# Kernel tuning notes

Measured on AMD Instinct MI355X. Metric: run time of the kernel, lower is better.

## Reference

```python
import jax, jax.numpy as jnp
import numpy as np

BATCH = 1024


def setup_inputs() -> dict:
    key = jax.random.key(0)
    ks = jax.random.split(key, 8)
    piece_positions = jax.random.randint(ks[0], (BATCH, 64, 10), 0, 2) > 0  # bool occupancy
    king_positions = jax.random.randint(ks[1], (BATCH, 2), 0, 64, dtype=jnp.int32)
    input_weights = jax.random.randint(ks[2], (64, 641, 256), -32768, 32767, dtype=jnp.int16)
    input_bias = jnp.zeros((256,), dtype=jnp.int16)
    w1 = jax.random.randint(ks[3], (32, 512), -128, 127, dtype=jnp.int8)
    b1 = jnp.zeros((32,), dtype=jnp.int32)
    w2 = jax.random.randint(ks[4], (32, 32), -128, 127, dtype=jnp.int8)
    b2 = jnp.zeros((32,), dtype=jnp.int32)
    out_w = jax.random.randint(ks[5], (32,), -128, 127, dtype=jnp.int8)
    out_b = jnp.zeros((1,), dtype=jnp.int32)
    return {
        'piece_positions': piece_positions, 'king_positions': king_positions,
        'input_weights': input_weights, 'input_bias': input_bias,
        'w1': w1, 'b1': b1, 'w2': w2, 'b2': b2, 'out_w': out_w, 'out_b': out_b,
    }


def _fc(x, w, b):
    # int8 inputs/weights, int32 accumulate, floor-div 64, clamp to [0,127] -> int8
    y = x.astype(jnp.int32) @ w.T.astype(jnp.int32) + b
    y = jnp.floor_divide(y, 64)
    return jnp.clip(y, 0, 127).astype(jnp.int8)


def reference(piece_positions, king_positions, input_weights, input_bias,
              w1, b1, w2, b2, out_w, out_b):
    B = piece_positions.shape[0]
    pp = piece_positions.reshape(B, 640).astype(jnp.int32)  # flattened 64x10 HalfKP features

    def half(king_idx):
        wk = input_weights[king_idx]            # (B, 641, 256) gathered per-sample king table
        feats = wk[:, :640, :].astype(jnp.int32)
        kbias = wk[:, 640, :].astype(jnp.int32)
        return jnp.einsum('bf,bfd->bd', pp, feats) + kbias  # (B, 256)

    white = half(king_positions[:, 0])
    black = half(king_positions[:, 1])
    # int16 wraparound semantics of the original: accumulate in int32, mod-cast to int16
    acc = (white + black + input_bias.astype(jnp.int32)).astype(jnp.int16)

    x = jnp.clip(acc, 0, 127).astype(jnp.int8)
    x = jnp.concatenate([x, x], axis=1)  # (B, 512) side_to_move || other_side
    x = _fc(x, w1, b1)
    x = _fc(x, w2, b2)
    s = jnp.sum(x.astype(jnp.int32) * out_w.astype(jnp.int32)) + out_b  # scalar sum over batch too (as in source)
    return jnp.floor_divide(s, 16)  # shape (1,)
```

## Files before the change

kernel.cpp:

```cpp
#include <hip/hip_runtime.h>
#include <stdint.h>

#define NDIM  256
#define NFEAT 640
#define NROWS 641
#define SG    8
#define GSTRIDE 4
#define MAXRPB 320
#define CPB   4
#define MAXSLOTS 2048

typedef unsigned short ushort4v __attribute__((ext_vector_type(4)));
typedef unsigned short ushort8v __attribute__((ext_vector_type(8)));

struct GatherLds {
    int flags[2];
    int cnt;
    unsigned short list[MAXSLOTS];
    int samp[SG];
    int slotid[SG];
    unsigned mask[MAXRPB];
    unsigned red[4][SG][NDIM / 2];
};

template<bool RAWW, bool RAWPP>
__device__ __forceinline__ void gather_body(
    const void* __restrict__ ppv, const void* __restrict__ Wv,
    unsigned short* __restrict__ partial, int nslots, int rp, GatherLds& sh)
{
    const int bid = blockIdx.x;
    const int k = bid & 63;
    const int rest = bid >> 6;
    const int p = rest & (rp - 1);
    const int g0 = rest >> (rp == 4 ? 2 : 1);
    const int t = threadIdx.x, l = t & 63, g = t >> 6;

    const int cnt = sh.cnt;
    const int rpb = NFEAT / rp;
    const int r0 = p * rpb;
    const int rows_per_wave = rpb / 4;
    const int lbeg = g * rows_per_wave;
    const char* Wk = (const char*)Wv + (size_t)k * NROWS * NDIM * (RAWW ? 2 : 4);

    for (int gi = g0; gi * SG < cnt; gi += GSTRIDE) {
        const int base = gi * SG;
        const int ns = min(SG, cnt - base);
        const unsigned emask = (1u << ns) - 1u;

        if (t < SG) {
            const int s = sh.list[base + min(t, ns - 1)];
            sh.slotid[t] = s;
            sh.samp[t] = s >> 1;
        }
        __syncthreads();

        for (int r = t; r < rpb; r += 256) {
            unsigned mm = 0;
            #pragma unroll
            for (int i = 0; i < SG; ++i) {
                const int s = sh.samp[i];
                int v;
                if (RAWPP) v = ((const uint8_t*)ppv)[(size_t)s * NFEAT + r0 + r];
                else       v = ((const int*)ppv)[(size_t)s * NFEAT + r0 + r];
                mm |= (v != 0 ? 1u : 0u) << i;
            }
            sh.mask[r] = mm & emask;
        }
        __syncthreads();

        ushort4v acc[SG];
        #pragma unroll
        for (int i = 0; i < SG; ++i) acc[i] = (ushort4v)0;

        #pragma unroll 2
        for (int rr = 0; rr < rows_per_wave; ++rr) {
            const int lr = lbeg + rr;
            unsigned mm = sh.mask[lr];
            mm = __builtin_amdgcn_readfirstlane(mm);
            ushort4v w;
            if (RAWW) {
                w = *(const ushort4v*)(Wk + (size_t)(r0 + lr) * 512 + (size_t)l * 8);
            } else {
                const int4 u = *(const int4*)(Wk + (size_t)(r0 + lr) * 1024 + (size_t)l * 16);
                w.x = (unsigned short)u.x; w.y = (unsigned short)u.y;
                w.z = (unsigned short)u.z; w.w = (unsigned short)u.w;
            }
            #pragma unroll
            for (int i = 0; i < SG; ++i)
                if (mm & (1u << i)) acc[i] += w;
        }

        #pragma unroll
        for (int i = 0; i < SG; ++i)
            *(ushort4v*)&sh.red[g][i][2 * l] = acc[i];
        __syncthreads();

        const int i = t >> 5;
        const int j4 = (t & 31) * 4;
        if (i < ns) {
            ushort8v sv = *(const ushort8v*)&sh.red[0][i][j4];
            #pragma unroll
            for (int g2 = 1; g2 < 4; ++g2) sv += *(const ushort8v*)&sh.red[g2][i][j4];
            *(ushort8v*)&partial[((size_t)p * nslots + sh.slotid[i]) * NDIM + (size_t)(t & 31) * 8] = sv;
        }
        __syncthreads();
    }
}

__global__ __launch_bounds__(256, 4) void nnue_gather(
    const void* __restrict__ pp, const int* __restrict__ kp,
    const void* __restrict__ W, unsigned short* __restrict__ partial,
    int* __restrict__ ws, int nslots, int rp)
{
    __shared__ GatherLds sh;
    const int t = threadIdx.x, l = t & 63, g = t >> 6;
    const int k = blockIdx.x & 63;

    if (blockIdx.x == 0 && t == 0) { ws[0] = 0; ws[3] = 0; }

    if (t == 0) {
        int raww = 0, rawpp = 0;
        const int* W32 = (const int*)W;
        const int* pp32 = (const int*)pp;
        for (int i = 0; i < 16; ++i) {
            const int v = W32[i];
            if (v > 32767 || v < -32768) raww = 1;
            const int u = pp32[i];
            if (u != 0 && u != 1) rawpp = 1;
        }
        sh.flags[0] = raww; sh.flags[1] = rawpp;
    }
    if (g == 0) {
        int cnt = 0;
        for (int c = 0; c < nslots; c += 64) {
            const int s = c + l;
            const bool f = (s < nslots) && (kp[s] == k);
            const unsigned long long m = __ballot(f);
            if (f) sh.list[cnt + (int)__popcll(m & ((1ull << l) - 1ull))] = (unsigned short)s;
            cnt += (int)__popcll(m);
        }
        if (l == 0) sh.cnt = cnt;
    }
    __syncthreads();

    const int raww = sh.flags[0], rawpp = sh.flags[1];
    if (raww) {
        if (rawpp) gather_body<true,  true >(pp, W, partial, nslots, rp, sh);
        else       gather_body<true,  false>(pp, W, partial, nslots, rp, sh);
    } else {
        if (rawpp) gather_body<false, true >(pp, W, partial, nslots, rp, sh);
        else       gather_body<false, false>(pp, W, partial, nslots, rp, sh);
    }
}

struct CombineLds {
    alignas(16) int8_t x[NDIM];
    int fc[256];
    alignas(4) int8_t x2[32];
    int flags;
};

template<bool RAWW>
__device__ __forceinline__ void combine_body(
    const unsigned short* __restrict__ partial, const int* __restrict__ kp,
    const void* __restrict__ Wv, const void* __restrict__ ibv,
    const void* __restrict__ w1v, const int* __restrict__ b1,
    const void* __restrict__ w2v, const int* __restrict__ b2,
    const void* __restrict__ owv, const int* __restrict__ ob,
    int* __restrict__ ws, int* __restrict__ out,
    int nslots, int B, int rp, CombineLds& sh)
{
    const int t = threadIdx.x;
    int blocksum = 0;

    for (int ss = 0; ss < CPB; ++ss) {
        const int b = blockIdx.x * CPB + ss;
        if (b >= B) break;
        const int k0 = kp[2 * b + 0];
        const int k1 = kp[2 * b + 1];
        {
            unsigned tot = 0;
            for (int pi = 0; pi < rp; ++pi) {
                tot += partial[((size_t)pi * nslots + 2 * b + 0) * NDIM + t];
                tot += partial[((size_t)pi * nslots + 2 * b + 1) * NDIM + t];
            }
            if (RAWW) {
                const uint16_t* Wq = (const uint16_t*)Wv;
                tot += Wq[((size_t)k0 * NROWS + NFEAT) * NDIM + t];
                tot += Wq[((size_t)k1 * NROWS + NFEAT) * NDIM + t];
                tot += ((const uint16_t*)ibv)[t];
            } else {
                const int* Wq = (const int*)Wv;
                tot += (unsigned)Wq[((size_t)k0 * NROWS + NFEAT) * NDIM + t];
                tot += (unsigned)Wq[((size_t)k1 * NROWS + NFEAT) * NDIM + t];
                tot += (unsigned)((const int*)ibv)[t];
            }
            int v = (int)(int16_t)(uint16_t)tot;
            v = v < 0 ? 0 : (v > 127 ? 127 : v);
            sh.x[t] = (int8_t)v;
        }
        __syncthreads();

        {
            const int o = t >> 3, part = t & 7;
            int y = 0;
            const uint32_t* xw = (const uint32_t*)sh.x;
            if (RAWW) {
                const uint32_t* w1r = (const uint32_t*)((const char*)w1v + o * 512);
                #pragma unroll
                for (int i = 0; i < 8; ++i) {
                    const int wi = part * 8 + i;
                    const uint32_t xv = xw[wi];
                    const uint32_t wa = w1r[wi];
                    const uint32_t wb = w1r[64 + wi];
                    #pragma unroll
                    for (int jj = 0; jj < 4; ++jj) {
                        const int xj  = (int)((xv >> (8 * jj)) & 0xFFu);
                        const int waj = (int)(int8_t)(uint8_t)(wa >> (8 * jj));
                        const int wbj = (int)(int8_t)(uint8_t)(wb >> (8 * jj));
                        y += xj * (waj + wbj);
                    }
                }
            } else {
                const int* w1r = (const int*)w1v + o * 512;
                #pragma unroll
                for (int i = 0; i < 8; ++i) {
                    const int wi = part * 8 + i;
                    const uint32_t xv = xw[wi];
                    #pragma unroll
                    for (int jj = 0; jj < 4; ++jj) {
                        const int xj = (int)((xv >> (8 * jj)) & 0xFFu);
                        y += xj * (w1r[wi * 4 + jj] + w1r[256 + wi * 4 + jj]);
                    }
                }
            }
            sh.fc[t] = y;
        }
        __syncthreads();

        if (t < 32) {
            int y = b1[t];
            #pragma unroll
            for (int pq = 0; pq < 8; ++pq) y += sh.fc[t * 8 + pq];
            y >>= 6;
            y = y < 0 ? 0 : (y > 127 ? 127 : y);
            sh.x2[t] = (int8_t)y;
        }
        __syncthreads();

        if (t < 32) {
            int y = b2[t];
            const uint32_t* x2w = (const uint32_t*)sh.x2;
            if (RAWW) {
                const uint32_t* w2r = (const uint32_t*)((const char*)w2v + t * 32);
                #pragma unroll
                for (int i = 0; i < 8; ++i) {
                    const uint32_t xv = x2w[i];
                    const uint32_t wv = w2r[i];
                    #pragma unroll
                    for (int jj = 0; jj < 4; ++jj)
                        y += (int)((xv >> (8 * jj)) & 0xFFu) * (int)(int8_t)(uint8_t)(wv >> (8 * jj));
                }
            } else {
                const int* w2r = (const int*)w2v + t * 32;
                #pragma unroll
                for (int i = 0; i < 8; ++i) {
                    const uint32_t xv = x2w[i];
                    #pragma unroll
                    for (int jj = 0; jj < 4; ++jj)
                        y += (int)((xv >> (8 * jj)) & 0xFFu) * w2r[i * 4 + jj];
                }
            }
            y >>= 6;
            y = y < 0 ? 0 : (y > 127 ? 127 : y);
            const int owx = RAWW ? (int)((const int8_t*)owv)[t] : ((const int*)owv)[t];
            int pr = y * owx;
            #pragma unroll
            for (int off = 16; off > 0; off >>= 1) pr += __shfl_down(pr, off, 32);
            if (t == 0) blocksum += pr;
        }
        __syncthreads();
    }

    if (t == 0) {
        atomicAdd(&ws[0], blocksum);
        __threadfence();
        const int ticket = atomicAdd(&ws[3], 1);
        if (ticket == (int)gridDim.x - 1) {
            const int s = atomicAdd(&ws[0], 0);
            out[0] = (s + ob[0]) >> 4;
        }
    }
}

__global__ __launch_bounds__(256) void nnue_combine(
    const unsigned short* __restrict__ partial, const int* __restrict__ kp,
    const void* __restrict__ W, const void* __restrict__ ib,
    const void* __restrict__ w1, const int* __restrict__ b1,
    const void* __restrict__ w2, const int* __restrict__ b2,
    const void* __restrict__ ow, const int* __restrict__ ob,
    int* __restrict__ ws, int* __restrict__ out, int nslots, int B, int rp)
{
    __shared__ CombineLds sh;
    if (threadIdx.x == 0) {
        int raww = 0;
        const int* W32 = (const int*)W;
        for (int i = 0; i < 16; ++i) {
            const int v = W32[i];
            if (v > 32767 || v < -32768) raww = 1;
        }
        sh.flags = raww;
    }
    __syncthreads();
    if (sh.flags) combine_body<true >(partial, kp, W, ib, w1, b1, w2, b2, ow, ob, ws, out, nslots, B, rp, sh);
    else          combine_body<false>(partial, kp, W, ib, w1, b1, w2, b2, ow, ob, ws, out, nslots, B, rp, sh);
}

__global__ void nnue_finalize(const int* __restrict__ ws, const int* __restrict__ ob,
                              int* __restrict__ out) {
    out[0] = (ws[0] + ob[0]) >> 4;
}

struct SharedBuf {
    uint8_t pp[NFEAT];
    int     acc[4][NDIM];
    alignas(16) int8_t x[NDIM];
    int     fc[256];
    alignas(4) int8_t x2[32];
    int     list[4][160];
};

__global__ void detect_layout(const int* __restrict__ W32, const int* __restrict__ pp32,
                              int* __restrict__ ws) {
    int raww = 0, rawpp = 0;
    for (int i = 0; i < 16; ++i) {
        const int v = W32[i];
        if (v > 32767 || v < -32768) raww = 1;
        const int u = pp32[i];
        if (u != 0 && u != 1) rawpp = 1;
    }
    ws[0] = 0; ws[1] = raww; ws[2] = rawpp;
}

template<bool RAWW, bool RAWPP>
__device__ __forceinline__ void mono_body(
    const void* __restrict__ ppv, const int* __restrict__ kp,
    const void* __restrict__ Wv,  const void* __restrict__ ibv,
    const void* __restrict__ w1v, const int* __restrict__ b1,
    const void* __restrict__ w2v, const int* __restrict__ b2,
    const void* __restrict__ owv, int* __restrict__ ws, SharedBuf& sh)
{
    const int b = blockIdx.x;
    const int t = threadIdx.x;
    const int l = t & 63;
    const int g = t >> 6;

    if (RAWPP) {
        const uint32_t* src = (const uint32_t*)((const uint8_t*)ppv + (size_t)b * NFEAT);
        if (t < NFEAT / 4) ((uint32_t*)sh.pp)[t] = src[t];
    } else {
        const int* src = (const int*)ppv + (size_t)b * NFEAT;
        for (int i = t; i < NFEAT; i += 256) sh.pp[i] = (uint8_t)(src[i] != 0);
    }
    __syncthreads();

    const int base = g * 160;
    int cnt = 0;
    for (int c = 0; c < 160; c += 64) {
        const int idx = c + l;
        const bool flag = (idx < 160) && (sh.pp[base + idx] != 0);
        const unsigned long long mmask = __ballot(flag);
        const int pos = cnt + (int)__popcll(mmask & ((1ull << l) - 1ull));
        if (flag) sh.list[g][pos] = base + idx;
        cnt += (int)__popcll(mmask);
    }

    const int k0 = kp[b * 2 + 0];
    const int k1 = kp[b * 2 + 1];
    int a0 = 0, a1 = 0, a2 = 0, a3 = 0, a4 = 0, a5 = 0, a6 = 0, a7 = 0;

    if (RAWW) {
        const char* W0 = (const char*)Wv + (size_t)k0 * (NROWS * NDIM * 2);
        const char* W1 = (const char*)Wv + (size_t)k1 * (NROWS * NDIM * 2);
        const int lo = l * 8;
        auto step = [&](int f) {
            const uint2 u0 = *(const uint2*)(W0 + f * 512 + lo);
            const uint2 u1 = *(const uint2*)(W1 + f * 512 + lo);
            a0 += (int)(u0.x & 0xFFFFu); a1 += (int)(u0.x >> 16);
            a2 += (int)(u0.y & 0xFFFFu); a3 += (int)(u0.y >> 16);
            a4 += (int)(u1.x & 0xFFFFu); a5 += (int)(u1.x >> 16);
            a6 += (int)(u1.y & 0xFFFFu); a7 += (int)(u1.y >> 16);
        };
        int j = 0;
        for (; j + 4 <= cnt; j += 4) {
            const int f0 = sh.list[g][j], f1 = sh.list[g][j + 1];
            const int f2 = sh.list[g][j + 2], f3 = sh.list[g][j + 3];
            step(f0); step(f1); step(f2); step(f3);
        }
        for (; j < cnt; ++j) step(sh.list[g][j]);
    } else {
        const char* W0 = (const char*)Wv + (size_t)k0 * (NROWS * NDIM * 4);
        const char* W1 = (const char*)Wv + (size_t)k1 * (NROWS * NDIM * 4);
        const int lo = l * 16;
        auto step = [&](int f) {
            const int4 u0 = *(const int4*)(W0 + f * 1024 + lo);
            const int4 u1 = *(const int4*)(W1 + f * 1024 + lo);
            a0 += u0.x; a1 += u0.y; a2 += u0.z; a3 += u0.w;
            a4 += u1.x; a5 += u1.y; a6 += u1.z; a7 += u1.w;
        };
        int j = 0;
        for (; j + 4 <= cnt; j += 4) {
            const int f0 = sh.list[g][j], f1 = sh.list[g][j + 1];
            const int f2 = sh.list[g][j + 2], f3 = sh.list[g][j + 3];
            step(f0); step(f1); step(f2); step(f3);
        }
        for (; j < cnt; ++j) step(sh.list[g][j]);
    }

    sh.acc[g][4 * l + 0] = a0 + a4;
    sh.acc[g][4 * l + 1] = a1 + a5;
    sh.acc[g][4 * l + 2] = a2 + a6;
    sh.acc[g][4 * l + 3] = a3 + a7;
    __syncthreads();

    {
        const int d = t;
        int tot = sh.acc[0][d] + sh.acc[1][d] + sh.acc[2][d] + sh.acc[3][d];
        int kb0, kb1, ibx;
        if (RAWW) {
            const int16_t* Wq = (const int16_t*)Wv;
            kb0 = Wq[((size_t)k0 * NROWS + NFEAT) * NDIM + d];
            kb1 = Wq[((size_t)k1 * NROWS + NFEAT) * NDIM + d];
            ibx = ((const int16_t*)ibv)[d];
        } else {
            const int* Wq = (const int*)Wv;
            kb0 = Wq[((size_t)k0 * NROWS + NFEAT) * NDIM + d];
            kb1 = Wq[((size_t)k1 * NROWS + NFEAT) * NDIM + d];
            ibx = ((const int*)ibv)[d];
        }
        tot += kb0 + kb1 + ibx;
        int v = (int)(int16_t)(uint16_t)(uint32_t)tot;
        v = v < 0 ? 0 : (v > 127 ? 127 : v);
        sh.x[d] = (int8_t)v;
    }
    __syncthreads();

    {
        const int o = t >> 3, part = t & 7;
        int y = 0;
        const uint32_t* xw = (const uint32_t*)sh.x;
        if (RAWW) {
            const uint32_t* w1r = (const uint32_t*)((const char*)w1v + o * 512);
            #pragma unroll
            for (int i = 0; i < 8; ++i) {
                const int wi = part * 8 + i;
                const uint32_t xv = xw[wi];
                const uint32_t wa = w1r[wi];
                const uint32_t wb = w1r[64 + wi];
                #pragma unroll
                for (int jj = 0; jj < 4; ++jj) {
                    const int xj  = (int)((xv >> (8 * jj)) & 0xFFu);
                    const int waj = (int)(int8_t)(uint8_t)(wa >> (8 * jj));
                    const int wbj = (int)(int8_t)(uint8_t)(wb >> (8 * jj));
                    y += xj * (waj + wbj);
                }
            }
        } else {
            const int* w1r = (const int*)w1v + o * 512;
            #pragma unroll
            for (int i = 0; i < 8; ++i) {
                const int wi = part * 8 + i;
                const uint32_t xv = xw[wi];
                #pragma unroll
                for (int jj = 0; jj < 4; ++jj) {
                    const int xj = (int)((xv >> (8 * jj)) & 0xFFu);
                    y += xj * (w1r[wi * 4 + jj] + w1r[256 + wi * 4 + jj]);
                }
            }
        }
        sh.fc[t] = y;
    }
    __syncthreads();

    if (t < 32) {
        int y = b1[t];
        #pragma unroll
        for (int pq = 0; pq < 8; ++pq) y += sh.fc[t * 8 + pq];
        y >>= 6;
        y = y < 0 ? 0 : (y > 127 ? 127 : y);
        sh.x2[t] = (int8_t)y;
    }
    __syncthreads();

    if (t < 32) {
        int y = b2[t];
        const uint32_t* x2w = (const uint32_t*)sh.x2;
        if (RAWW) {
            const uint32_t* w2r = (const uint32_t*)((const char*)w2v + t * 32);
            #pragma unroll
            for (int i = 0; i < 8; ++i) {
                const uint32_t xv = x2w[i];
                const uint32_t wv = w2r[i];
                #pragma unroll
                for (int jj = 0; jj < 4; ++jj)
                    y += (int)((xv >> (8 * jj)) & 0xFFu) * (int)(int8_t)(uint8_t)(wv >> (8 * jj));
            }
        } else {
            const int* w2r = (const int*)w2v + t * 32;
            #pragma unroll
            for (int i = 0; i < 8; ++i) {
                const uint32_t xv = x2w[i];
                #pragma unroll
                for (int jj = 0; jj < 4; ++jj)
                    y += (int)((xv >> (8 * jj)) & 0xFFu) * w2r[i * 4 + jj];
            }
        }
        y >>= 6;
        y = y < 0 ? 0 : (y > 127 ? 127 : y);
        const int owx = RAWW ? (int)((const int8_t*)owv)[t] : ((const int*)owv)[t];
        int pr = y * owx;
        #pragma unroll
        for (int off = 16; off > 0; off >>= 1) pr += __shfl_down(pr, off, 32);
        if (t == 0) atomicAdd(ws, pr);
    }
}

__global__ __launch_bounds__(256, 4) void nnue_mono(
    const void* __restrict__ pp, const int* __restrict__ kp,
    const void* __restrict__ W,  const void* __restrict__ ib,
    const void* __restrict__ w1, const int* __restrict__ b1,
    const void* __restrict__ w2, const int* __restrict__ b2,
    const void* __restrict__ ow, int* __restrict__ ws)
{
    __shared__ SharedBuf sh;
    const int raww = ws[1], rawpp = ws[2];
    if (raww) {
        if (rawpp) mono_body<true,  true >(pp, kp, W, ib, w1, b1, w2, b2, ow, ws, sh);
        else       mono_body<true,  false>(pp, kp, W, ib, w1, b1, w2, b2, ow, ws, sh);
    } else {
        if (rawpp) mono_body<false, true >(pp, kp, W, ib, w1, b1, w2, b2, ow, ws, sh);
        else       mono_body<false, false>(pp, kp, W, ib, w1, b1, w2, b2, ow, ws, sh);
    }
}

extern "C" void kernel_launch(void* const* d_in, const int* in_sizes, int n_in,
                              void* d_out, int out_size, void* d_ws, size_t ws_size,
                              hipStream_t stream)
{
    const void* pp = d_in[0];
    const int*  kp = (const int*)d_in[1];
    const void* W  = d_in[2];
    const void* ib = d_in[3];
    const void* w1 = d_in[4];
    const int*  b1 = (const int*)d_in[5];
    const void* w2 = d_in[6];
    const int*  b2 = (const int*)d_in[7];
    const void* ow = d_in[8];
    const int*  ob = (const int*)d_in[9];
    int* ws  = (int*)d_ws;
    int* out = (int*)d_out;

    const int B = in_sizes[1] / 2;
    const int nslots = 2 * B;

    const size_t off_pb = 256;
    const size_t need4 = (off_pb + (size_t)4 * nslots * (NDIM / 2)) * 4;
    const size_t need2 = (off_pb + (size_t)2 * nslots * (NDIM / 2)) * 4;

    int rp = 0;
    if (ws_size >= need4) rp = 4;
    else if (ws_size >= need2) rp = 2;

    if (rp && nslots <= MAXSLOTS) {
        unsigned short* partial = (unsigned short*)(ws + off_pb);
        hipLaunchKernelGGL(nnue_gather, dim3(64 * rp * GSTRIDE), dim3(256), 0, stream,
                           pp, kp, W, partial, ws, nslots, rp);
        hipLaunchKernelGGL(nnue_combine, dim3((B + CPB - 1) / CPB), dim3(256), 0, stream,
                           partial, kp, W, ib, w1, b1, w2, b2, ow, ob, ws, out, nslots, B, rp);
    } else {
        hipLaunchKernelGGL(detect_layout, dim3(1), dim3(1), 0, stream,
                           (const int*)W, (const int*)pp, ws);
        hipLaunchKernelGGL(nnue_mono, dim3(B), dim3(256), 0, stream,
                           pp, kp, W, ib, w1, b1, w2, b2, ow, ws);
        hipLaunchKernelGGL(nnue_finalize, dim3(1), dim3(1), 0, stream, ws, ob, out);
    }
}
```

Before: 161.8 us.

## Fuse bucket, gather and combine into one cooperative kernel with per-wave work units

Replaces the two-kernel gather/combine path with a single cooperative-launch kernel. It bucket-sorts slots by king index into global workspace, then does a grid sync, a gather phase, another grid sync and a combine phase. The gather is restructured so each wave owns an independent (partition, sample-group) unit with its own LDS mask. This drops the cross-wave LDS reduction and the block barriers, and the weight loads are unrolled by four rows. The aim is to cut launch overhead and barrier stalls, at the cost of grid-wide syncs and one wave redundantly re-reading pp for its own rows. A three-kernel fallback is kept for when cooperative launch is unavailable.

```diff
diff --git a/kernel.cpp b/kernel.cpp
--- a/kernel.cpp
+++ b/kernel.cpp
@@ -1,181 +1,171 @@
 #include <hip/hip_runtime.h>
+#include <hip/hip_cooperative_groups.h>
 #include <stdint.h>
+
+namespace cg = cooperative_groups;
 
 #define NDIM  256
 #define NFEAT 640
 #define NROWS 641
 #define SG    8
-#define GSTRIDE 4
-#define MAXRPB 320
-#define CPB   4
+#define KCAP  2048
 #define MAXSLOTS 2048
+#define GRID_MAIN 1024
+#define OFF_KCNT  8
+#define OFF_KLIST 128
+#define OFF_PART  (OFF_KLIST + 64 * KCAP)
 
 typedef unsigned short ushort4v __attribute__((ext_vector_type(4)));
-typedef unsigned short ushort8v __attribute__((ext_vector_type(8)));
-
-struct GatherLds {
-    int flags[2];
-    int cnt;
-    unsigned short list[MAXSLOTS];
-    int samp[SG];
-    int slotid[SG];
-    unsigned mask[MAXRPB];
-    unsigned red[4][SG][NDIM / 2];
+
+struct FusedLds {
+    union {
+        unsigned mask[4][320];
+        struct { alignas(16) int8_t x[NDIM]; int fc[256]; alignas(4) int8_t x2[32]; } c;
+        int bcnt;
+    };
 };
 
+__device__ __forceinline__ void detect_flags(const void* W, const void* pp,
+                                             int* raww, int* rawpp)
+{
+    int a = 0, b = 0;
+    const int* W32 = (const int*)W;
+    const int* pp32 = (const int*)pp;
+    for (int i = 0; i < 16; ++i) {
+        const int v = W32[i];
+        if (v > 32767 || v < -32768) a = 1;
+        const int u = pp32[i];
+        if (u != 0 && u != 1) b = 1;
+    }
+    *raww = a; *rawpp = b;
+}
+
+__device__ __forceinline__ void bucket_phase(const int* __restrict__ kp, int nslots,
+                                             int* __restrict__ kcnt, int* __restrict__ klist,
+                                             int* __restrict__ bcnt)
+{
+    const int bid = blockIdx.x, t = threadIdx.x;
+    if (bid >= 64) return;
+    if (t == 0) *bcnt = 0;
+    __syncthreads();
+    for (int s = t; s < nslots; s += 256) {
+        if (kp[s] == bid) {
+            const int pos = atomicAdd(bcnt, 1);
+            if (pos < KCAP) klist[bid * KCAP + pos] = s;
+        }
+    }
+    __syncthreads();
+    if (t == 0) kcnt[bid] = (*bcnt > KCAP) ? KCAP : *bcnt;
+}
+
 template<bool RAWW, bool RAWPP>
-__device__ __forceinline__ void gather_body(
+__device__ __forceinline__ void gather_phase(
     const void* __restrict__ ppv, const void* __restrict__ Wv,
-    unsigned short* __restrict__ partial, int nslots, int rp, GatherLds& sh)
+    const int* __restrict__ kcnt, const int* __restrict__ klist,
+    unsigned short* __restrict__ partial, int nslots, int rp,
+    unsigned* __restrict__ maskbase)
 {
     const int bid = blockIdx.x;
     const int k = bid & 63;
-    const int rest = bid >> 6;
-    const int p = rest & (rp - 1);
-    const int g0 = rest >> (rp == 4 ? 2 : 1);
     const int t = threadIdx.x, l = t & 63, g = t >> 6;
-
-    const int cnt = sh.cnt;
+    const int nwv = (gridDim.x >> 6) << 2;
+    const int wv0 = ((bid >> 6) << 2) + g;
+    unsigned* mym = maskbase + g * 320;
+
+    const int cnt = kcnt[k];
+    if (cnt <= 0) return;
+    const int gmax = (cnt + SG - 1) >> 3;
+    const int nunits = rp * gmax;
     const int rpb = NFEAT / rp;
-    const int r0 = p * rpb;
-    const int rows_per_wave = rpb / 4;
-    const int lbeg = g * rows_per_wave;
+    const int pshift = (rp == 4) ? 2 : 1;
     const char* Wk = (const char*)Wv + (size_t)k * NROWS * NDIM * (RAWW ? 2 : 4);
-
-    for (int gi = g0; gi * SG < cnt; gi += GSTRIDE) {
+    const int* kl = klist + k * KCAP;
+
+    for (int u = wv0; u < nunits; u += nwv) {
+        const int p = u & (rp - 1);
+        const int gi = u >> pshift;
         const int base = gi * SG;
         const int ns = min(SG, cnt - base);
-        const unsigned emask = (1u << ns) - 1u;
-
-        if (t < SG) {
-            const int s = sh.list[base + min(t, ns - 1)];
-            sh.slotid[t] = s;
-            sh.samp[t] = s >> 1;
-        }
-        __syncthreads();
-
-        for (int r = t; r < rpb; r += 256) {
+        const int r0 = p * rpb;
+
+        int slots[SG], samps[SG];
+        #pragma unroll
+        for (int i = 0; i < SG; ++i) {
+            const int s = kl[base + (i < ns ? i : ns - 1)];
+            slots[i] = s; samps[i] = s >> 1;
+        }
+
+        for (int r = l; r < rpb; r += 64) {
             unsigned mm = 0;
             #pragma unroll
             for (int i = 0; i < SG; ++i) {
-                const int s = sh.samp[i];
                 int v;
-                if (RAWPP) v = ((const uint8_t*)ppv)[(size_t)s * NFEAT + r0 + r];
-                else       v = ((const int*)ppv)[(size_t)s * NFEAT + r0 + r];
+                if (RAWPP) v = ((const uint8_t*)ppv)[(size_t)samps[i] * NFEAT + r0 + r];
+                else       v = ((const int*)ppv)[(size_t)samps[i] * NFEAT + r0 + r];
                 mm |= (v != 0 ? 1u : 0u) << i;
             }
-            sh.mask[r] = mm & emask;
-        }
-        __syncthreads();
+            mym[r] = (ns < SG) ? (mm & ((1u << ns) - 1u)) : mm;
+        }
+        asm volatile("s_waitcnt lgkmcnt(0)" ::: "memory");
 
         ushort4v acc[SG];
         #pragma unroll
         for (int i = 0; i < SG; ++i) acc[i] = (ushort4v)0;
 
-        #pragma unroll 2
-        for (int rr = 0; rr < rows_per_wave; ++rr) {
-            const int lr = lbeg + rr;
-            unsigned mm = sh.mask[lr];
-            mm = __builtin_amdgcn_readfirstlane(mm);
-            ushort4v w;
-            if (RAWW) {
-                w = *(const ushort4v*)(Wk + (size_t)(r0 + lr) * 512 + (size_t)l * 8);
+        const char* rb = Wk + (size_t)r0 * (RAWW ? 512 : 1024) + (size_t)l * (RAWW ? 8 : 16);
+        const int rstep = RAWW ? 2048 : 4096;
+        for (int r = 0; r < rpb; r += 4, rb += rstep) {
+            ushort4v w0, w1, w2, w3;
+            if constexpr (RAWW) {
+                w0 = *(const ushort4v*)(rb);
+                w1 = *(const ushort4v*)(rb + 512);
+                w2 = *(const ushort4v*)(rb + 1024);
+                w3 = *(const ushort4v*)(rb + 1536);
             } else {
-                const int4 u = *(const int4*)(Wk + (size_t)(r0 + lr) * 1024 + (size_t)l * 16);
-                w.x = (unsigned short)u.x; w.y = (unsigned short)u.y;
-                w.z = (unsigned short)u.z; w.w = (unsigned short)u.w;
-            }
-            #pragma unroll
-            for (int i = 0; i < SG; ++i)
-                if (mm & (1u << i)) acc[i] += w;
+                const int4 u0 = *(const int4*)(rb);
+                const int4 u1 = *(const int4*)(rb + 1024);
+                const int4 u2 = *(const int4*)(rb + 2048);
+                const int4 u3 = *(const int4*)(rb + 3072);
+                w0.x=(unsigned short)u0.x; w0.y=(unsigned short)u0.y; w0.z=(unsigned short)u0.z; w0.w=(unsigned short)u0.w;
+                w1.x=(unsigned short)u1.x; w1.y=(unsigned short)u1.y; w1.z=(unsigned short)u1.z; w1.w=(unsigned short)u1.w;
+                w2.x=(unsigned short)u2.x; w2.y=(unsigned short)u2.y; w2.z=(unsigned short)u2.z; w2.w=(unsigned short)u2.w;
+                w3.x=(unsigned short)u3.x; w3.y=(unsigned short)u3.y; w3.z=(unsigned short)u3.z; w3.w=(unsigned short)u3.w;
+            }
+            unsigned m0 = mym[r+0], m1 = mym[r+1], m2 = mym[r+2], m3 = mym[r+3];
+            m0 = __builtin_amdgcn_readfirstlane(m0);
+            m1 = __builtin_amdgcn_readfirstlane(m1);
+            m2 = __builtin_amdgcn_readfirstlane(m2);
+            m3 = __builtin_amdgcn_readfirstlane(m3);
+            #pragma unroll
+            for (int i = 0; i < SG; ++i) {
+                if (m0 & (1u << i)) acc[i] += w0;
+                if (m1 & (1u << i)) acc[i] += w1;
+                if (m2 & (1u << i)) acc[i] += w2;
+                if (m3 & (1u << i)) acc[i] += w3;
+            }
         }
 
         #pragma unroll
         for (int i = 0; i < SG; ++i)
-            *(ushort4v*)&sh.red[g][i][2 * l] = acc[i];
-        __syncthreads();
-
-        const int i = t >> 5;
-        const int j4 = (t & 31) * 4;
-        if (i < ns) {
-            ushort8v sv = *(const ushort8v*)&sh.red[0][i][j4];
-            #pragma unroll
-            for (int g2 = 1; g2 < 4; ++g2) sv += *(const ushort8v*)&sh.red[g2][i][j4];
-            *(ushort8v*)&partial[((size_t)p * nslots + sh.slotid[i]) * NDIM + (size_t)(t & 31) * 8] = sv;
-        }
-        __syncthreads();
-    }
-}
-
-__global__ __launch_bounds__(256, 4) void nnue_gather(
-    const void* __restrict__ pp, const int* __restrict__ kp,
-    const void* __restrict__ W, unsigned short* __restrict__ partial,
-    int* __restrict__ ws, int nslots, int rp)
-{
-    __shared__ GatherLds sh;
-    const int t = threadIdx.x, l = t & 63, g = t >> 6;
-    const int k = blockIdx.x & 63;
-
-    if (blockIdx.x == 0 && t == 0) { ws[0] = 0; ws[3] = 0; }
-
-    if (t == 0) {
-        int raww = 0, rawpp = 0;
-        const int* W32 = (const int*)W;
-        const int* pp32 = (const int*)pp;
-        for (int i = 0; i < 16; ++i) {
-            const int v = W32[i];
-            if (v > 32767 || v < -32768) raww = 1;
-            const int u = pp32[i];
-            if (u != 0 && u != 1) rawpp = 1;
-        }
-        sh.flags[0] = raww; sh.flags[1] = rawpp;
-    }
-    if (g == 0) {
-        int cnt = 0;
-        for (int c = 0; c < nslots; c += 64) {
-            const int s = c + l;
-            const bool f = (s < nslots) && (kp[s] == k);
-            const unsigned long long m = __ballot(f);
-            if (f) sh.list[cnt + (int)__popcll(m & ((1ull << l) - 1ull))] = (unsigned short)s;
-            cnt += (int)__popcll(m);
-        }
-        if (l == 0) sh.cnt = cnt;
-    }
-    __syncthreads();
-
-    const int raww = sh.flags[0], rawpp = sh.flags[1];
-    if (raww) {
-        if (rawpp) gather_body<true,  true >(pp, W, partial, nslots, rp, sh);
-        else       gather_body<true,  false>(pp, W, partial, nslots, rp, sh);
-    } else {
-        if (rawpp) gather_body<false, true >(pp, W, partial, nslots, rp, sh);
-        else       gather_body<false, false>(pp, W, partial, nslots, rp, sh);
-    }
-}
-
-struct CombineLds {
-    alignas(16) int8_t x[NDIM];
-    int fc[256];
-    alignas(4) int8_t x2[32];
-    int flags;
-};
+            if (i < ns)
+                *(ushort4v*)&partial[((size_t)p * nslots + slots[i]) * NDIM + (size_t)l * 4] = acc[i];
+    }
+}
 
 template<bool RAWW>
-__device__ __forceinline__ void combine_body(
+__device__ __forceinline__ void combine_phase(
     const unsigned short* __restrict__ partial, const int* __restrict__ kp,
     const void* __restrict__ Wv, const void* __restrict__ ibv,
     const void* __restrict__ w1v, const int* __restrict__ b1,
     const void* __restrict__ w2v, const int* __restrict__ b2,
     const void* __restrict__ owv, const int* __restrict__ ob,
     int* __restrict__ ws, int* __restrict__ out,
-    int nslots, int B, int rp, CombineLds& sh)
+    int nslots, int B, int rp, FusedLds& sh)
 {
     const int t = threadIdx.x;
     int blocksum = 0;
 
-    for (int ss = 0; ss < CPB; ++ss) {
-        const int b = blockIdx.x * CPB + ss;
-        if (b >= B) break;
+    for (int b = blockIdx.x; b < B; b += gridDim.x) {
         const int k0 = kp[2 * b + 0];
         const int k1 = kp[2 * b + 1];
         {
@@ -197,14 +187,14 @@
             }
             int v = (int)(int16_t)(uint16_t)tot;
             v = v < 0 ? 0 : (v > 127 ? 127 : v);
-            sh.x[t] = (int8_t)v;
+            sh.c.x[t] = (int8_t)v;
         }
         __syncthreads();
 
         {
             const int o = t >> 3, part = t & 7;
             int y = 0;
-            const uint32_t* xw = (const uint32_t*)sh.x;
+            const uint32_t* xw = (const uint32_t*)sh.c.x;
             if (RAWW) {
                 const uint32_t* w1r = (const uint32_t*)((const char*)w1v + o * 512);
                 #pragma unroll
@@ -234,23 +224,23 @@
                     }
                 }
             }
-            sh.fc[t] = y;
+            sh.c.fc[t] = y;
         }
         __syncthreads();
 
         if (t < 32) {
             int y = b1[t];
             #pragma unroll
-            for (int pq = 0; pq < 8; ++pq) y += sh.fc[t * 8 + pq];
+            for (int pq = 0; pq < 8; ++pq) y += sh.c.fc[t * 8 + pq];
             y >>= 6;
             y = y < 0 ? 0 : (y > 127 ? 127 : y);
-            sh.x2[t] = (int8_t)y;
+            sh.c.x2[t] = (int8_t)y;
         }
         __syncthreads();
 
         if (t < 32) {
             int y = b2[t];
-            const uint32_t* x2w = (const uint32_t*)sh.x2;
+            const uint32_t* x2w = (const uint32_t*)sh.c.x2;
             if (RAWW) {
                 const uint32_t* w2r = (const uint32_t*)((const char*)w2v + t * 32);
                 #pragma unroll
@@ -282,43 +272,101 @@
         __syncthreads();
     }
 
-    if (t == 0) {
+    const int nticket = (int)gridDim.x < B ? (int)gridDim.x : B;
+    if (t == 0 && (int)blockIdx.x < nticket) {
         atomicAdd(&ws[0], blocksum);
         __threadfence();
         const int ticket = atomicAdd(&ws[3], 1);
-        if (ticket == (int)gridDim.x - 1) {
+        if (ticket == nticket - 1) {
             const int s = atomicAdd(&ws[0], 0);
             out[0] = (s + ob[0]) >> 4;
         }
     }
 }
 
-__global__ __launch_bounds__(256) void nnue_combine(
-    const unsigned short* __restrict__ partial, const int* __restrict__ kp,
-    const void* __restrict__ W, const void* __restrict__ ib,
+__global__ __launch_bounds__(256, 4) void nnue_fused(
+    const void* __restrict__ pp, const int* __restrict__ kp,
+    const void* __restrict__ W,  const void* __restrict__ ib,
+    const void* __restrict__ w1, const int* __restrict__ b1,
+    const void* __restrict__ w2, const int* __restrict__ b2,
+    const void* __restrict__ ow, const int* __restrict__ ob,
+    int* __restrict__ ws, int* __restrict__ out,
+    int nslots, int B, int rp)
+{
+    __shared__ FusedLds sh;
+    __shared__ int s_raww, s_rawpp;
+    const int t = threadIdx.x;
+    if (t == 0) {
+        detect_flags(W, pp, &s_raww, &s_rawpp);
+        if (blockIdx.x == 0) { ws[0] = 0; ws[3] = 0; }
+    }
+    __syncthreads();
+    const int raww = s_raww, rawpp = s_rawpp;
+
+    int* kcnt  = ws + OFF_KCNT;
+    int* klist = ws + OFF_KLIST;
+    unsigned short* partial = (unsigned short*)(ws + OFF_PART);
+
+    bucket_phase(kp, nslots, kcnt, klist, &sh.bcnt);
+    cg::this_grid().sync();
+
+    if (raww) {
+        if (rawpp) gather_phase<true,  true >(pp, W, kcnt, klist, partial, nslots, rp, &sh.mask[0][0]);
+        else       gather_phase<true,  false>(pp, W, kcnt, klist, partial, nslots, rp, &sh.mask[0][0]);
+    } else {
+        if (rawpp) gather_phase<false, true >(pp, W, kcnt, klist, partial, nslots, rp, &sh.mask[0][0]);
+        else       gather_phase<false, false>(pp, W, kcnt, klist, partial, nslots, rp, &sh.mask[0][0]);
+    }
+    cg::this_grid().sync();
+
+    if (raww) combine_phase<true >(partial, kp, W, ib, w1, b1, w2, b2, ow, ob, ws, out, nslots, B, rp, sh);
+    else      combine_phase<false>(partial, kp, W, ib, w1, b1, w2, b2, ow, ob, ws, out, nslots, B, rp, sh);
+}
+
+__global__ __launch_bounds__(256) void k_bucket(const int* __restrict__ kp,
+                                                int* __restrict__ ws, int nslots)
+{
+    __shared__ int bcnt;
+    if (blockIdx.x == 0 && threadIdx.x == 0) { ws[0] = 0; ws[3] = 0; }
+    bucket_phase(kp, nslots, ws + OFF_KCNT, ws + OFF_KLIST, &bcnt);
+}
+
+__global__ __launch_bounds__(256, 4) void k_gather(
+    const void* __restrict__ pp, const void* __restrict__ W,
+    int* __restrict__ ws, int nslots, int rp)
+{
+    __shared__ FusedLds sh;
+    __shared__ int s_raww, s_rawpp;
+    if (threadIdx.x == 0) detect_flags(W, pp, &s_raww, &s_rawpp);
+    __syncthreads();
+    const int raww = s_raww, rawpp = s_rawpp;
+    int* kcnt  = ws + OFF_KCNT;
+    int* klist = ws + OFF_KLIST;
+    unsigned short* partial = (unsigned short*)(ws + OFF_PART);
+    if (raww) {
+        if (rawpp) gather_phase<true,  true >(pp, W, kcnt, klist, partial, nslots, rp, &sh.mask[0][0]);
+        else       gather_phase<true,  false>(pp, W, kcnt, klist, partial, nslots, rp, &sh.mask[0][0]);
+    } else {
+        if (rawpp) gather_phase<false, true >(pp, W, kcnt, klist, partial, nslots, rp, &sh.mask[0][0]);
+        else       gather_phase<false, false>(pp, W, kcnt, klist, partial, nslots, rp, &sh.mask[0][0]);
+    }
+}
+
+__global__ __launch_bounds__(256) void k_combine(
+    const int* __restrict__ kp, const void* __restrict__ pp, const void* __restrict__ W,
+    const void* __restrict__ ib,
     const void* __restrict__ w1, const int* __restrict__ b1,
     const void* __restrict__ w2, const int* __restrict__ b2,
     const void* __restrict__ ow, const int* __restrict__ ob,
     int* __restrict__ ws, int* __restrict__ out, int nslots, int B, int rp)
 {
-    __shared__ CombineLds sh;
-    if (threadIdx.x == 0) {
-        int raww = 0;
-        const int* W32 = (const int*)W;
-        for (int i = 0; i < 16; ++i) {
-            const int v = W32[i];
-            if (v > 32767 || v < -32768) raww = 1;
-        }
-        sh.flags = raww;
-    }
-    __syncthreads();
-    if (sh.flags) combine_body<true >(partial, kp, W, ib, w1, b1, w2, b2, ow, ob, ws, out, nslots, B, rp, sh);
-    else          combine_body<false>(partial, kp, W, ib, w1, b1, w2, b2, ow, ob, ws, out, nslots, B, rp, sh);
-}
-
-__global__ void nnue_finalize(const int* __restrict__ ws, const int* __restrict__ ob,
-                              int* __restrict__ out) {
-    out[0] = (ws[0] + ob[0]) >> 4;
+    __shared__ FusedLds sh;
+    __shared__ int s_raww, s_rawpp;
+    if (threadIdx.x == 0) detect_flags(W, pp, &s_raww, &s_rawpp);
+    __syncthreads();
+    unsigned short* partial = (unsigned short*)(ws + OFF_PART);
+    if (s_raww) combine_phase<true >(partial, kp, W, ib, w1, b1, w2, b2, ow, ob, ws, out, nslots, B, rp, sh);
+    else        combine_phase<false>(partial, kp, W, ib, w1, b1, w2, b2, ow, ob, ws, out, nslots, B, rp, sh);
 }
 
 struct SharedBuf {
@@ -332,13 +380,8 @@
 
 __global__ void detect_layout(const int* __restrict__ W32, const int* __restrict__ pp32,
                               int* __restrict__ ws) {
-    int raww = 0, rawpp = 0;
-    for (int i = 0; i < 16; ++i) {
-        const int v = W32[i];
-        if (v > 32767 || v < -32768) raww = 1;
-        const int u = pp32[i];
-        if (u != 0 && u != 1) rawpp = 1;
-    }
+    int raww, rawpp;
+    detect_flags(W32, pp32, &raww, &rawpp);
     ws[0] = 0; ws[1] = raww; ws[2] = rawpp;
 }
 
@@ -543,6 +586,11 @@
     }
 }
 
+__global__ void nnue_finalize(const int* __restrict__ ws, const int* __restrict__ ob,
+                              int* __restrict__ out) {
+    out[0] = (ws[0] + ob[0]) >> 4;
+}
+
 extern "C" void kernel_launch(void* const* d_in, const int* in_sizes, int n_in,
                               void* d_out, int out_size, void* d_ws, size_t ws_size,
                               hipStream_t stream)
@@ -563,25 +611,48 @@
     const int B = in_sizes[1] / 2;
     const int nslots = 2 * B;
 
-    const size_t off_pb = 256;
-    const size_t need4 = (off_pb + (size_t)4 * nslots * (NDIM / 2)) * 4;
-    const size_t need2 = (off_pb + (size_t)2 * nslots * (NDIM / 2)) * 4;
-
+    const size_t need4 = ((size_t)OFF_PART + (size_t)4 * nslots * (NDIM / 2)) * 4;
+    const size_t need2 = ((size_t)OFF_PART + (size_t)2 * nslots * (NDIM / 2)) * 4;
     int rp = 0;
     if (ws_size >= need4) rp = 4;
     else if (ws_size >= need2) rp = 2;
 
-    if (rp && nslots <= MAXSLOTS) {
-        unsigned short* partial = (unsigned short*)(ws + off_pb);
-        hipLaunchKernelGGL(nnue_gather, dim3(64 * rp * GSTRIDE), dim3(256), 0, stream,
-                           pp, kp, W, partial, ws, nslots, rp);
-        hipLaunchKernelGGL(nnue_combine, dim3((B + CPB - 1) / CPB), dim3(256), 0, stream,
-                           partial, kp, W, ib, w1, b1, w2, b2, ow, ob, ws, out, nslots, B, rp);
-    } else {
-        hipLaunchKernelGGL(detect_layout, dim3(1), dim3(1), 0, stream,
-                           (const int*)W, (const int*)pp, ws);
-        hipLaunchKernelGGL(nnue_mono, dim3(B), dim3(256), 0, stream,
-                           pp, kp, W, ib, w1, b1, w2, b2, ow, ws);
-        hipLaunchKernelGGL(nnue_finalize, dim3(1), dim3(1), 0, stream, ws, ob, out);
-    }
-}
+    if (rp && nslots <= MAXSLOTS && B > 0) {
+        static int grid_coop = -2;
+        if (grid_coop == -2) {
+            int dev = 0; hipGetDevice(&dev);
+            int coop = 0; hipDeviceGetAttribute(&coop, hipDeviceAttributeCooperativeLaunch, dev);
+            int ncu = 0;  hipDeviceGetAttribute(&ncu, hipDeviceAttributeMultiprocessorCount, dev);
+            int nb = 0;
+            hipError_t oe = hipOccupancyMaxActiveBlocksPerMultiprocessor(&nb, nnue_fused, 256, 0);
+            if (coop && oe == hipSuccess && nb > 0 && ncu > 0) {
+                int gmax = ((nb * ncu) / 64) * 64;
+                grid_coop = (gmax >= 64) ? (gmax < GRID_MAIN ? gmax : GRID_MAIN) : -1;
+            } else {
+                grid_coop = -1;
+            }
+        }
+        int nslots_arg = nslots, B_arg = B, rp_arg = rp;
+        if (grid_coop > 0) {
+            void* args[] = {(void*)&pp, (void*)&kp, (void*)&W, (void*)&ib,
+                            (void*)&w1, (void*)&b1, (void*)&w2, (void*)&b2,
+                            (void*)&ow, (void*)&ob, (void*)&ws, (void*)&out,
+                            (void*)&nslots_arg, (void*)&B_arg, (void*)&rp_arg};
+            hipError_t e = hipLaunchCooperativeKernel(nnue_fused, dim3(grid_coop), dim3(256),
+                                                      args, 0, stream);
+            if (e == hipSuccess) return;
+            grid_coop = -1;
+        }
+        hipLaunchKernelGGL(k_bucket, dim3(64), dim3(256), 0, stream, kp, ws, nslots);
+        hipLaunchKernelGGL(k_gather, dim3(GRID_MAIN), dim3(256), 0, stream, pp, W, ws, nslots, rp);
+        hipLaunchKernelGGL(k_combine, dim3(GRID_MAIN), dim3(256), 0, stream,
+                           kp, pp, W, ib, w1, b1, w2, b2, ow, ob, ws, out, nslots, B, rp);
+        return;
+    }
+
+    hipLaunchKernelGGL(detect_layout, dim3(1), dim3(1), 0, stream,
+                       (const int*)W, (const int*)pp, ws);
+    hipLaunchKernelGGL(nnue_mono, dim3(B), dim3(256), 0, stream,
+                       pp, kp, W, ib, w1, b1, w2, b2, ow, ws);
+    hipLaunchKernelGGL(nnue_finalize, dim3(1), dim3(1), 0, stream, ws, ob, out);
+}
```

Result: slower. 262.7 us (+62.4%).
